# Kernel optimization log

Measured on AMD Instinct MI355X. Metric: run time of the kernel, lower is better.

The kernel has to match this reference:

```python
import jax, jax.numpy as jnp
import numpy as np

S = 3072        # total packed tokens
E = 1280        # d_model
H = 20          # encoder_attention_heads
D = E // H      # head_dim = 64
NSEG = 16       # number of packed audio chunks


def setup_inputs() -> dict:
    key = jax.random.key(0)
    ks = jax.random.split(key, 9)
    w = lambda k, shape: (jax.random.normal(k, shape, jnp.float32) * 0.02)
    hidden_states = jax.random.normal(ks[0], (S, E), jnp.float32)
    cu_seqlens = (jnp.arange(NSEG + 1, dtype=jnp.int32) * (S // NSEG))
    return {
        "hidden_states": hidden_states,
        "Wq": w(ks[1], (E, E)), "bq": w(ks[2], (E,)),
        "Wk": w(ks[3], (E, E)),                      # k_proj has no bias
        "Wv": w(ks[4], (E, E)), "bv": w(ks[5], (E,)),
        "Wo": w(ks[6], (E, E)), "bo": w(ks[7], (E,)),
        "cu_seqlens": cu_seqlens,
    }


def reference(hidden_states, Wq, bq, Wk, Wv, bv, Wo, bo, cu_seqlens):
    Sq, Em = hidden_states.shape
    Dh = Em // H
    # projections (torch Linear: x @ W.T + b)
    q = (hidden_states @ Wq.T + bq).reshape(Sq, H, Dh).transpose(1, 0, 2)  # [H,S,D]
    k = (hidden_states @ Wk.T).reshape(Sq, H, Dh).transpose(1, 0, 2)       # [H,S,D]
    v = (hidden_states @ Wv.T + bv).reshape(Sq, H, Dh).transpose(1, 0, 2)  # [H,S,D]
    # block-diagonal additive mask from cu_seqlens (vectorized equivalent of
    # the original Python loop): tokens attend only within their own segment.
    pos = jnp.arange(Sq)
    seg = jnp.searchsorted(cu_seqlens[1:], pos, side="right")              # segment id per token
    same = seg[:, None] == seg[None, :]                                    # [S,S]
    bias = jnp.where(same, 0.0, jnp.finfo(q.dtype).min)
    attn = jnp.einsum("hqd,hkd->hqk", q, k) / np.sqrt(Dh).astype(q.dtype)  # [H,S,S]
    attn = jax.nn.softmax(attn + bias, axis=-1)
    out = jnp.einsum("hqk,hkd->hqd", attn, v)                              # [H,S,D]
    out = out.transpose(1, 0, 2).reshape(Sq, Em)
    return out @ Wo.T + bo
```

## Files before the change

kernel.cpp:

```cpp
#include <hip/hip_runtime.h>
#include <hip/hip_bf16.h>
#include <stdint.h>

#define S_TOK 3072
#define E_DIM 1280
#define H_NUM 20
#define D_HEAD 64
#define NSEG 16

typedef __attribute__((ext_vector_type(8))) short short8;
typedef __attribute__((ext_vector_type(4))) float f32x4;

__device__ __forceinline__ unsigned short f2bf(float f){
  union { float f; unsigned int i; } u; u.f = f;
  unsigned int r = u.i + 0x7FFFu + ((u.i >> 16) & 1u);
  return (unsigned short)(r >> 16);
}

__device__ __forceinline__ void gload_lds16(const void* g, void* l){
  __builtin_amdgcn_global_load_lds((__attribute__((address_space(1))) void*)(g),
                                   (__attribute__((address_space(3))) void*)(l), 16, 0, 0);
}

__global__ void cvt_all(const float* __restrict__ hs,
                        const float* __restrict__ w0, const float* __restrict__ w1,
                        const float* __restrict__ w2,
                        unsigned short* __restrict__ hsb,
                        unsigned short* __restrict__ dqkv,
                        int nHS4, int nW4){
  int i = blockIdx.x * blockDim.x + threadIdx.x;
  const float* src;
  unsigned short* dst;
  size_t sj, dj;
  if (i < nHS4){
    src = hs; dst = hsb; sj = i; dj = i;
  } else {
    int t = i - nHS4;
    int w = t / nW4;
    if (w >= 3) return;
    int j = t - w * nW4;
    src = (w == 0) ? w0 : (w == 1) ? w1 : w2;
    sj = j;
    dst = dqkv; dj = (size_t)w * nW4 + j;
  }
  float4 v = reinterpret_cast<const float4*>(src)[sj];
  ushort4 o;
  o.x = f2bf(v.x); o.y = f2bf(v.y); o.z = f2bf(v.z); o.w = f2bf(v.w);
  reinterpret_cast<ushort4*>(dst)[dj] = o;
}

#define LGKM0 do { asm volatile("s_waitcnt lgkmcnt(0)" ::: "memory");         \
                   __builtin_amdgcn_sched_barrier(0); } while (0)
#define BAR   __builtin_amdgcn_s_barrier()

__global__ __launch_bounds__(512, 2) void gemm_qkv(
    const unsigned short* __restrict__ A,
    const unsigned short* __restrict__ Bp,
    const float* __restrict__ bias0,
    const float* __restrict__ bias1,
    unsigned short* __restrict__ Oq,
    unsigned short* __restrict__ Ok,
    unsigned short* __restrict__ Ov,
    int K)
{
  constexpr int SLOT = (192 + 256) * 64;
  __shared__ __align__(16) unsigned short SH[2 * SLOT];

  const int nwg = gridDim.x;
  const int xcd = blockIdx.x & 7, ix = blockIdx.x >> 3;
  const int wg = xcd * (nwg >> 3) + ix;
  const int st = wg / 20, ii = wg % 20;
  const int bm = (st / 3) * 4 + ii / 5;
  const int bn = (st % 3) * 5 + ii % 5;
  const int row0 = bm * 192, col0 = bn * 256;

  const int tid  = threadIdx.x;
  const int lane = tid & 63;
  const int w    = tid >> 6;
  const int wm   = w >> 2;
  const int wn   = w & 3;

  const f32x4 fz = {0.f, 0.f, 0.f, 0.f};
  f32x4 acc[4][3][2];
#pragma unroll
  for (int qd = 0; qd < 4; ++qd)
#pragma unroll
    for (int m = 0; m < 3; ++m)
#pragma unroll
      for (int n = 0; n < 2; ++n) acc[qd][m][n] = fz;

  auto stA = [&](int t){
    unsigned short* d = SH + (t & 1) * SLOT;
    const unsigned short* g = A + (size_t)row0 * K + (t << 6);
#pragma unroll
    for (int i = 0; i < 3; ++i){
      int s = i * 512 + tid;
      int r = s >> 3, ks = (s & 7) ^ (r & 7);
      gload_lds16(g + (size_t)r * K + ks * 8, d + s * 8);
    }
  };
  auto stB = [&](int h, int t){
    unsigned short* d = SH + (t & 1) * SLOT + 12288 + h * 8192;
    const unsigned short* g = Bp + (size_t)(col0 + h * 128) * K + (t << 6);
#pragma unroll
    for (int i = 0; i < 2; ++i){
      int s = i * 512 + tid;
      int r = s >> 3, ks = (s & 7) ^ (r & 7);
      gload_lds16(g + (size_t)r * K + ks * 8, d + s * 8);
    }
  };

  short8 af[3][2], bf0[2][2], bf1[2][2];
  auto RA = [&](int mh, int db){
    const unsigned short* Ah = SH + db * SLOT;
#pragma unroll
    for (int m = 0; m < 3; ++m){
      int ra = mh * 96 + wm * 48 + m * 16 + (lane & 15);
#pragma unroll
      for (int kk = 0; kk < 2; ++kk){
        int sl = kk * 4 + (lane >> 4);
        af[m][kk] = *reinterpret_cast<const short8*>(&Ah[ra * 64 + ((sl ^ (ra & 7))) * 8]);
      }
    }
  };
  auto RB = [&](int nh, int db, short8 (*bf)[2]){
    const unsigned short* Bb = SH + db * SLOT + 12288;
#pragma unroll
    for (int n = 0; n < 2; ++n){
      int rb = nh * 128 + wn * 32 + n * 16 + (lane & 15);
#pragma unroll
      for (int kk = 0; kk < 2; ++kk){
        int sl = kk * 4 + (lane >> 4);
        bf[n][kk] = *reinterpret_cast<const short8*>(&Bb[rb * 64 + ((sl ^ (rb & 7))) * 8]);
      }
    }
  };

#define MF_Q(QD, BF)                                                          \
  do {                                                                        \
    __builtin_amdgcn_s_setprio(1);                                            \
    _Pragma("unroll")                                                         \
    for (int kk = 0; kk < 2; ++kk)                                            \
      _Pragma("unroll")                                                       \
      for (int m = 0; m < 3; ++m)                                             \
        _Pragma("unroll")                                                     \
        for (int n = 0; n < 2; ++n)                                           \
          acc[QD][m][n] = __builtin_amdgcn_mfma_f32_16x16x32_bf16(            \
              af[m][kk], BF[n][kk], acc[QD][m][n], 0, 0, 0);                  \
    __builtin_amdgcn_s_setprio(0);                                            \
  } while (0)

  const int nk = K >> 6;
  stA(0); stB(0, 0); stB(1, 0);
  for (int t = 0; t < nk; ++t){
    const int db = t & 1;
    const bool nx = (t + 1 < nk);
    asm volatile("s_waitcnt vmcnt(2)" ::: "memory");
    BAR;
    RA(0, db); RB(0, db, bf0);
    if (nx) stA(t + 1);
    LGKM0; MF_Q(0, bf0);
    if (nx) asm volatile("s_waitcnt vmcnt(3)" ::: "memory");
    else    asm volatile("s_waitcnt vmcnt(0)" ::: "memory");
    BAR;
    RB(1, db, bf1);
    if (nx) stB(0, t + 1);
    LGKM0; MF_Q(1, bf1);
    BAR;
    RA(1, db);
    if (nx) stB(1, t + 1);
    LGKM0; MF_Q(2, bf1);
    BAR;
    MF_Q(3, bf0);
  }
  __syncthreads();

  {
    unsigned short* Cs = SH;
    const int CSTR = 264;
    const int mat = col0 / E_DIM;
    const int cc0 = col0 - mat * E_DIM;
    unsigned short* dst = (mat == 0) ? Oq : ((mat == 1) ? Ok : Ov);
    float bb[2][2];
#pragma unroll
    for (int nh = 0; nh < 2; ++nh)
#pragma unroll
      for (int n = 0; n < 2; ++n){
        int cc = cc0 + nh * 128 + wn * 32 + n * 16 + (lane & 15);
        bb[nh][n] = (mat == 0) ? bias0[cc] : (mat == 2 ? bias1[cc] : 0.0f);
      }
#pragma unroll
    for (int ph = 0; ph < 2; ++ph){
#pragma unroll
      for (int q2i = 0; q2i < 2; ++q2i){
        const int qd = ph * 2 + q2i;
        const int nh = (qd >> 1) ^ (qd & 1);
#pragma unroll
        for (int m = 0; m < 3; ++m)
#pragma unroll
          for (int n = 0; n < 2; ++n)
#pragma unroll
            for (int j = 0; j < 4; ++j){
              int rr = wm * 48 + m * 16 + (lane >> 4) * 4 + j;
              int c  = nh * 128 + wn * 32 + n * 16 + (lane & 15);
              Cs[rr * CSTR + c] = f2bf(acc[qd][m][n][j] + bb[nh][n]);
            }
      }
      __syncthreads();
#pragma unroll
      for (int i = 0; i < 6; ++i){
        int tk  = i * 512 + tid;
        int p   = tk / 768;
        int idx = tk - p * 768;
        int rr  = idx >> 3, sq = idx & 7;
        short8 vv = *reinterpret_cast<const short8*>(&Cs[rr * CSTR + p * 64 + sq * 8]);
        int gr = row0 + ph * 96 + rr;
        int hh = (cc0 >> 6) + p;
        *reinterpret_cast<short8*>(&dst[((size_t)hh * S_TOK + gr) * D_HEAD + sq * 8]) = vv;
      }
      __syncthreads();
    }
  }
#undef MF_Q
}

__global__ __launch_bounds__(512, 2) void gemm_out(
    const unsigned short* __restrict__ A,
    const unsigned short* __restrict__ Bp,
    const float* __restrict__ bias0,
    float* __restrict__ Of,
    int K)
{
  constexpr int SLOT = 256 * 64;
  __shared__ __align__(16) unsigned short SH[3 * SLOT];

  const int nwg = gridDim.x;
  const int xcd = blockIdx.x & 7, ix = blockIdx.x >> 3;
  const int wg = xcd * (nwg >> 3) + ix;
  const int st = wg / 20, ii = wg % 20;
  const int bm = (st / 2) * 4 + ii / 5;
  const int bn = (st % 2) * 5 + ii % 5;
  const int row0 = bm * 128, col0 = bn * 128;

  const int tid  = threadIdx.x;
  const int lane = tid & 63;
  const int w    = tid >> 6;
  const int wm   = w >> 2;
  const int wn   = w & 3;

  const f32x4 fz = {0.f, 0.f, 0.f, 0.f};
  f32x4 acc[4][2];
#pragma unroll
  for (int m = 0; m < 4; ++m)
#pragma unroll
    for (int n = 0; n < 2; ++n) acc[m][n] = fz;

  auto stage = [&](int sl, int t){
    unsigned short* base = SH + sl * SLOT;
    const int k0 = t << 6;
#pragma unroll
    for (int i = 0; i < 4; ++i){
      int s = i * 512 + tid;
      int r = s >> 3, ks = (s & 7) ^ (r & 7);
      const unsigned short* g = (r < 128)
          ? A  + (size_t)(row0 + r) * K + k0 + ks * 8
          : Bp + (size_t)(col0 + (r - 128)) * K + k0 + ks * 8;
      gload_lds16(g, base + s * 8);
    }
  };

  const int nk = K >> 6;
  stage(0, 0);
  for (int t = 0; t < nk; ++t){
    if (t + 1 < nk){
      stage((t + 1) % 3, t + 1);
      asm volatile("s_waitcnt vmcnt(4)" ::: "memory");
    } else {
      asm volatile("s_waitcnt vmcnt(0)" ::: "memory");
    }
    BAR;
    const unsigned short* As = SH + (t % 3) * SLOT;
    const unsigned short* Bs = As + 128 * 64;
    short8 af[4][2], bf[2][2];
#pragma unroll
    for (int m = 0; m < 4; ++m){
      int ra = wm * 64 + m * 16 + (lane & 15);
#pragma unroll
      for (int kk = 0; kk < 2; ++kk){
        int sl = kk * 4 + (lane >> 4);
        af[m][kk] = *reinterpret_cast<const short8*>(&As[ra * 64 + ((sl ^ (ra & 7))) * 8]);
      }
    }
#pragma unroll
    for (int n = 0; n < 2; ++n){
      int rb = wn * 32 + n * 16 + (lane & 15);
#pragma unroll
      for (int kk = 0; kk < 2; ++kk){
        int sl = kk * 4 + (lane >> 4);
        bf[n][kk] = *reinterpret_cast<const short8*>(&Bs[rb * 64 + ((sl ^ (rb & 7))) * 8]);
      }
    }
    __builtin_amdgcn_s_setprio(1);
#pragma unroll
    for (int kk = 0; kk < 2; ++kk)
#pragma unroll
      for (int m = 0; m < 4; ++m)
#pragma unroll
        for (int n = 0; n < 2; ++n)
          acc[m][n] = __builtin_amdgcn_mfma_f32_16x16x32_bf16(af[m][kk], bf[n][kk], acc[m][n], 0, 0, 0);
    __builtin_amdgcn_s_setprio(0);
  }

  float bc[2];
#pragma unroll
  for (int n = 0; n < 2; ++n)
    bc[n] = bias0[col0 + wn * 32 + n * 16 + (lane & 15)];
#pragma unroll
  for (int m = 0; m < 4; ++m)
#pragma unroll
    for (int n = 0; n < 2; ++n){
      int c = col0 + wn * 32 + n * 16 + (lane & 15);
#pragma unroll
      for (int j = 0; j < 4; ++j){
        int r = row0 + wm * 64 + m * 16 + (lane >> 4) * 4 + j;
        Of[(size_t)r * E_DIM + c] = acc[m][n][j] + bc[n];
      }
    }
}

#define VSTR 200
#define PSTR 72
#define ATTN_BLKS (H_NUM * NSEG * 3)
__global__ __launch_bounds__(256, 3) void attn_kernel(
    const unsigned short* __restrict__ Q,
    const unsigned short* __restrict__ Kb,
    const unsigned short* __restrict__ V,
    const int* __restrict__ cu,
    unsigned short* __restrict__ O,
    const float* __restrict__ Wo,
    unsigned short* __restrict__ wob,
    int nW4)
{
  __shared__ __align__(16) unsigned short Vt[64*VSTR];
  __shared__ __align__(16) unsigned short Pw[4][16][PSTR];

  const int bid  = blockIdx.x;
  if (bid >= ATTN_BLKS){
    int i = (bid - ATTN_BLKS) * 256 + threadIdx.x;
    if (i < nW4){
      float4 v = reinterpret_cast<const float4*>(Wo)[i];
      ushort4 o;
      o.x = f2bf(v.x); o.y = f2bf(v.y); o.z = f2bf(v.z); o.w = f2bf(v.w);
      reinterpret_cast<ushort4*>(wob)[i] = o;
    }
    return;
  }
  const int unit = bid / 3;
  const int third= bid - unit*3;
  const int h    = unit >> 4;
  const int seg  = unit & 15;
  const int s0   = cu[seg];
  const int L    = cu[seg + 1] - s0;
  if (L <= 0) return;

  const int tid  = threadIdx.x;
  const int lane = tid & 63;
  const int w    = tid >> 6;
  const int row0g = third*64 + w*16;

  const unsigned short* qh = Q  + (size_t)h * S_TOK * D_HEAD;
  const unsigned short* kh = Kb + (size_t)h * S_TOK * D_HEAD;
  const unsigned short* vh = V  + (size_t)h * S_TOK * D_HEAD;

#pragma unroll
  for (int i = 0; i < 6; ++i){
    int task = i*256 + tid;
    int sr   = task % 192;
    int grp  = task / 192;
    int svr  = s0 + (sr < L ? sr : L - 1);
    short8 vv = *reinterpret_cast<const short8*>(vh + (size_t)svr*64 + grp*8);
#pragma unroll
    for (int j = 0; j < 8; ++j) Vt[(grp*8 + j)*VSTR + sr] = (unsigned short)vv[j];
  }

  short8 qf[2];
#pragma unroll
  for (int kk = 0; kk < 2; ++kk){
    int r  = row0g + (lane & 15);
    int sr = s0 + (r < L ? r : L - 1);
    qf[kk] = *reinterpret_cast<const short8*>(qh + (size_t)sr*64 + kk*32 + (lane >> 4)*8);
  }

  __syncthreads();

  const f32x4 fz = {0.f, 0.f, 0.f, 0.f};
  const float SCL = 0.125f * 1.44269504088896f;

  f32x4 sacc[12];
#pragma unroll
  for (int nt = 0; nt < 12; ++nt) sacc[nt] = fz;

#pragma unroll
  for (int nt = 0; nt < 12; ++nt){
    int rb = nt*16 + (lane & 15);
    int sr = s0 + (rb < L ? rb : L - 1);
    const unsigned short* kr = kh + (size_t)sr*64 + (lane >> 4)*8;
    short8 kf0 = *reinterpret_cast<const short8*>(kr);
    short8 kf1 = *reinterpret_cast<const short8*>(kr + 32);
    sacc[nt] = __builtin_amdgcn_mfma_f32_16x16x32_bf16(qf[0], kf0, sacc[nt], 0, 0, 0);
    sacc[nt] = __builtin_amdgcn_mfma_f32_16x16x32_bf16(qf[1], kf1, sacc[nt], 0, 0, 0);
  }

  float rinv[4];
#pragma unroll
  for (int j = 0; j < 4; ++j){
    float mx = -1e30f;
#pragma unroll
    for (int nt = 0; nt < 12; ++nt){
      int c = nt*16 + (lane & 15);
      float vv = (c < L) ? sacc[nt][j] : -1e30f;
      sacc[nt][j] = vv;
      mx = fmaxf(mx, vv);
    }
    mx = fmaxf(mx, __shfl_xor(mx, 1, 64));
    mx = fmaxf(mx, __shfl_xor(mx, 2, 64));
    mx = fmaxf(mx, __shfl_xor(mx, 4, 64));
    mx = fmaxf(mx, __shfl_xor(mx, 8, 64));
    float sum = 0.f;
#pragma unroll
    for (int nt = 0; nt < 12; ++nt){
      float pp = exp2f((sacc[nt][j] - mx) * SCL);
      sacc[nt][j] = pp;
      sum += pp;
    }
    sum += __shfl_xor(sum, 1, 64);
    sum += __shfl_xor(sum, 2, 64);
    sum += __shfl_xor(sum, 4, 64);
    sum += __shfl_xor(sum, 8, 64);
    rinv[j] = 1.0f / sum;
  }

  f32x4 oacc[4];
#pragma unroll
  for (int nt = 0; nt < 4; ++nt) oacc[nt] = fz;

#pragma unroll
  for (int kk = 0; kk < 6; ++kk){
#pragma unroll
    for (int ntl = 0; ntl < 2; ++ntl){
      int nt = kk*2 + ntl;
#pragma unroll
      for (int j = 0; j < 4; ++j)
        Pw[w][(lane >> 4)*4 + j][ntl*16 + (lane & 15)] = f2bf(sacc[nt][j]);
    }
    short8 pf = *reinterpret_cast<const short8*>(&Pw[w][lane & 15][(lane >> 4)*8]);
#pragma unroll
    for (int nt4 = 0; nt4 < 4; ++nt4){
      int dcol = nt4*16 + (lane & 15);
      short8 vf = *reinterpret_cast<const short8*>(&Vt[dcol*VSTR + kk*32 + (lane >> 4)*8]);
      oacc[nt4] = __builtin_amdgcn_mfma_f32_16x16x32_bf16(pf, vf, oacc[nt4], 0, 0, 0);
    }
  }

#pragma unroll
  for (int nt4 = 0; nt4 < 4; ++nt4)
#pragma unroll
    for (int j = 0; j < 4; ++j)
      Pw[w][(lane >> 4)*4 + j][nt4*16 + (lane & 15)] = f2bf(oacc[nt4][j] * rinv[j]);

  {
    int r = lane >> 2;
    int gr = row0g + r;
    if (gr < L){
#pragma unroll
      for (int part = 0; part < 2; ++part){
        int c0 = (lane & 3)*16 + part*8;
        short8 vv = *reinterpret_cast<const short8*>(&Pw[w][r][c0]);
        *reinterpret_cast<short8*>(&O[(size_t)(s0 + gr) * E_DIM + h*64 + c0]) = vv;
      }
    }
  }
}

extern "C" void kernel_launch(void* const* d_in, const int* in_sizes, int n_in,
                              void* d_out, int out_size, void* d_ws, size_t ws_size,
                              hipStream_t stream)
{
  const float* hs = (const float*)d_in[0];
  const float* Wq = (const float*)d_in[1];
  const float* bq = (const float*)d_in[2];
  const float* Wk = (const float*)d_in[3];
  const float* Wv = (const float*)d_in[4];
  const float* bv = (const float*)d_in[5];
  const float* Wo = (const float*)d_in[6];
  const float* bo = (const float*)d_in[7];
  const int*   cu = (const int*)d_in[8];
  float* out = (float*)d_out;

  unsigned short* p = (unsigned short*)d_ws;
  unsigned short* hsb  = p; p += (size_t)S_TOK * E_DIM;
  unsigned short* wqkv = p; p += (size_t)3 * E_DIM * E_DIM;
  unsigned short* wob  = p; p += (size_t)E_DIM * E_DIM;
  unsigned short* qb   = p; p += (size_t)S_TOK * E_DIM;
  unsigned short* kb   = p; p += (size_t)S_TOK * E_DIM;
  unsigned short* vb   = p; p += (size_t)S_TOK * E_DIM;
  unsigned short* aob  = p; p += (size_t)S_TOK * E_DIM;

  const int nHS4 = S_TOK * E_DIM / 4;
  const int nW4  = E_DIM * E_DIM / 4;
  const int nCvt = nHS4 + 3 * nW4;
  cvt_all<<<(nCvt + 255) / 256, 256, 0, stream>>>(hs, Wq, Wk, Wv, hsb, wqkv, nHS4, nW4);

  gemm_qkv<<<(S_TOK/192) * (3*E_DIM/256), 512, 0, stream>>>(
      hsb, wqkv, bq, bv, qb, kb, vb, E_DIM);

  const int cvtWoBlks = (nW4 + 255) / 256;
  attn_kernel<<<ATTN_BLKS + cvtWoBlks, 256, 0, stream>>>(
      qb, kb, vb, cu, aob, Wo, wob, nW4);

  gemm_out<<<(S_TOK/128) * (E_DIM/128), 512, 0, stream>>>(
      aob, wob, bo, out, E_DIM);
}
```

Measured before the change: 83.77 us.

## Fuse hidden-state bf16 conversion into QKV GEMM A-tile loads

Removes the separate fp32→bf16 conversion pass over the hidden states. The QKV GEMM now loads fp32 A tiles into registers, converts them with packed bf16 conversion instructions and writes them into LDS. B still uses async global-to-LDS loads. The fine-grained four-phase waitcnt and barrier schedule is replaced by a simpler one: a single sync per k-step, with the prefetch held in registers. This saves an intermediate round trip through global memory, but it doubles A read bytes inside the GEMM, adds register pressure, and gives up the async LDS load path for A.

```diff
diff --git a/kernel.cpp b/kernel.cpp
--- a/kernel.cpp
+++ b/kernel.cpp
@@ -22,31 +22,18 @@
                                    (__attribute__((address_space(3))) void*)(l), 16, 0, 0);
 }
 
-__global__ void cvt_all(const float* __restrict__ hs,
-                        const float* __restrict__ w0, const float* __restrict__ w1,
-                        const float* __restrict__ w2,
-                        unsigned short* __restrict__ hsb,
-                        unsigned short* __restrict__ dqkv,
-                        int nHS4, int nW4){
+__global__ void cvt_w(const float* __restrict__ w0, const float* __restrict__ w1,
+                      const float* __restrict__ w2,
+                      unsigned short* __restrict__ dqkv, int nW4){
   int i = blockIdx.x * blockDim.x + threadIdx.x;
-  const float* src;
-  unsigned short* dst;
-  size_t sj, dj;
-  if (i < nHS4){
-    src = hs; dst = hsb; sj = i; dj = i;
-  } else {
-    int t = i - nHS4;
-    int w = t / nW4;
-    if (w >= 3) return;
-    int j = t - w * nW4;
-    src = (w == 0) ? w0 : (w == 1) ? w1 : w2;
-    sj = j;
-    dst = dqkv; dj = (size_t)w * nW4 + j;
-  }
-  float4 v = reinterpret_cast<const float4*>(src)[sj];
+  int w = i / nW4;
+  if (w >= 3) return;
+  int j = i - w * nW4;
+  const float* src = (w == 0) ? w0 : (w == 1) ? w1 : w2;
+  float4 v = reinterpret_cast<const float4*>(src)[j];
   ushort4 o;
   o.x = f2bf(v.x); o.y = f2bf(v.y); o.z = f2bf(v.z); o.w = f2bf(v.w);
-  reinterpret_cast<ushort4*>(dst)[dj] = o;
+  reinterpret_cast<ushort4*>(dqkv)[(size_t)w * nW4 + j] = o;
 }
 
 #define LGKM0 do { asm volatile("s_waitcnt lgkmcnt(0)" ::: "memory");         \
@@ -54,7 +41,7 @@
 #define BAR   __builtin_amdgcn_s_barrier()
 
 __global__ __launch_bounds__(512, 2) void gemm_qkv(
-    const unsigned short* __restrict__ A,
+    const float* __restrict__ A,
     const unsigned short* __restrict__ Bp,
     const float* __restrict__ bias0,
     const float* __restrict__ bias1,
@@ -63,8 +50,7 @@
     unsigned short* __restrict__ Ov,
     int K)
 {
-  constexpr int SLOT = (192 + 256) * 64;
-  __shared__ __align__(16) unsigned short SH[2 * SLOT];
+  __shared__ __align__(16) unsigned short SH[57344];
 
   const int nwg = gridDim.x;
   const int xcd = blockIdx.x & 7, ix = blockIdx.x >> 3;
@@ -89,30 +75,42 @@
 #pragma unroll
       for (int n = 0; n < 2; ++n) acc[qd][m][n] = fz;
 
-  auto stA = [&](int t){
-    unsigned short* d = SH + (t & 1) * SLOT;
-    const unsigned short* g = A + (size_t)row0 * K + (t << 6);
+  float4 ar[3][2];
+  auto issueA = [&](int t){
+#pragma unroll
+    for (int i = 0; i < 3; ++i){
+      int s = i * 512 + tid, r = s >> 3, ks = (s & 7) ^ (r & 7);
+      const float* g = A + (size_t)(row0 + r) * K + (t << 6) + ks * 8;
+      ar[i][0] = *reinterpret_cast<const float4*>(g);
+      ar[i][1] = *reinterpret_cast<const float4*>(g + 4);
+    }
+  };
+  auto writeA = [&](int db){
+    unsigned short* dst = SH + db * 12288;
 #pragma unroll
     for (int i = 0; i < 3; ++i){
       int s = i * 512 + tid;
-      int r = s >> 3, ks = (s & 7) ^ (r & 7);
-      gload_lds16(g + (size_t)r * K + ks * 8, d + s * 8);
+      int4 o;
+      asm volatile("v_cvt_pk_bf16_f32 %0, %1, %2" : "=v"(o.x) : "v"(ar[i][0].x), "v"(ar[i][0].y));
+      asm volatile("v_cvt_pk_bf16_f32 %0, %1, %2" : "=v"(o.y) : "v"(ar[i][0].z), "v"(ar[i][0].w));
+      asm volatile("v_cvt_pk_bf16_f32 %0, %1, %2" : "=v"(o.z) : "v"(ar[i][1].x), "v"(ar[i][1].y));
+      asm volatile("v_cvt_pk_bf16_f32 %0, %1, %2" : "=v"(o.w) : "v"(ar[i][1].z), "v"(ar[i][1].w));
+      *reinterpret_cast<int4*>(dst + s * 8) = o;
     }
   };
-  auto stB = [&](int h, int t){
-    unsigned short* d = SH + (t & 1) * SLOT + 12288 + h * 8192;
-    const unsigned short* g = Bp + (size_t)(col0 + h * 128) * K + (t << 6);
-#pragma unroll
-    for (int i = 0; i < 2; ++i){
-      int s = i * 512 + tid;
-      int r = s >> 3, ks = (s & 7) ^ (r & 7);
+  auto stB = [&](int t){
+    unsigned short* d = SH + 24576 + (t & 1) * 16384;
+    const unsigned short* g = Bp + (size_t)col0 * K + (t << 6);
+#pragma unroll
+    for (int i = 0; i < 4; ++i){
+      int s = i * 512 + tid, r = s >> 3, ks = (s & 7) ^ (r & 7);
       gload_lds16(g + (size_t)r * K + ks * 8, d + s * 8);
     }
   };
 
   short8 af[3][2], bf0[2][2], bf1[2][2];
   auto RA = [&](int mh, int db){
-    const unsigned short* Ah = SH + db * SLOT;
+    const unsigned short* Ah = SH + db * 12288;
 #pragma unroll
     for (int m = 0; m < 3; ++m){
       int ra = mh * 96 + wm * 48 + m * 16 + (lane & 15);
@@ -124,7 +122,7 @@
     }
   };
   auto RB = [&](int nh, int db, short8 (*bf)[2]){
-    const unsigned short* Bb = SH + db * SLOT + 12288;
+    const unsigned short* Bb = SH + 24576 + db * 16384;
 #pragma unroll
     for (int n = 0; n < 2; ++n){
       int rb = nh * 128 + wn * 32 + n * 16 + (lane & 15);
@@ -151,26 +149,22 @@
   } while (0)
 
   const int nk = K >> 6;
-  stA(0); stB(0, 0); stB(1, 0);
+  issueA(0);
+  stB(0);
   for (int t = 0; t < nk; ++t){
     const int db = t & 1;
-    const bool nx = (t + 1 < nk);
-    asm volatile("s_waitcnt vmcnt(2)" ::: "memory");
-    BAR;
+    writeA(db);
+    __syncthreads();
+    if (t + 1 < nk){
+      stB(t + 1);
+      issueA(t + 1);
+    }
     RA(0, db); RB(0, db, bf0);
-    if (nx) stA(t + 1);
-    LGKM0; MF_Q(0, bf0);
-    if (nx) asm volatile("s_waitcnt vmcnt(3)" ::: "memory");
-    else    asm volatile("s_waitcnt vmcnt(0)" ::: "memory");
-    BAR;
+    MF_Q(0, bf0);
     RB(1, db, bf1);
-    if (nx) stB(0, t + 1);
-    LGKM0; MF_Q(1, bf1);
-    BAR;
+    MF_Q(1, bf1);
     RA(1, db);
-    if (nx) stB(1, t + 1);
-    LGKM0; MF_Q(2, bf1);
-    BAR;
+    MF_Q(2, bf1);
     MF_Q(3, bf0);
   }
   __syncthreads();
@@ -498,7 +492,6 @@
   float* out = (float*)d_out;
 
   unsigned short* p = (unsigned short*)d_ws;
-  unsigned short* hsb  = p; p += (size_t)S_TOK * E_DIM;
   unsigned short* wqkv = p; p += (size_t)3 * E_DIM * E_DIM;
   unsigned short* wob  = p; p += (size_t)E_DIM * E_DIM;
   unsigned short* qb   = p; p += (size_t)S_TOK * E_DIM;
@@ -506,13 +499,11 @@
   unsigned short* vb   = p; p += (size_t)S_TOK * E_DIM;
   unsigned short* aob  = p; p += (size_t)S_TOK * E_DIM;
 
-  const int nHS4 = S_TOK * E_DIM / 4;
   const int nW4  = E_DIM * E_DIM / 4;
-  const int nCvt = nHS4 + 3 * nW4;
-  cvt_all<<<(nCvt + 255) / 256, 256, 0, stream>>>(hs, Wq, Wk, Wv, hsb, wqkv, nHS4, nW4);
+  cvt_w<<<(3 * nW4 + 255) / 256, 256, 0, stream>>>(Wq, Wk, Wv, wqkv, nW4);
 
   gemm_qkv<<<(S_TOK/192) * (3*E_DIM/256), 512, 0, stream>>>(
-      hsb, wqkv, bq, bv, qb, kb, vb, E_DIM);
+      hs, wqkv, bq, bv, qb, kb, vb, E_DIM);
 
   const int cvtWoBlks = (nW4 + 255) / 256;
   attn_kernel<<<ATTN_BLKS + cvtWoBlks, 256, 0, stream>>>(
```

New measurement: 87.92 us. 5.0% more time.
